# Kernel tuning notes

Hardware: AMD Instinct MI355X
Metric: run time of the kernel (lower is better)

## Reference

```python
import jax, jax.numpy as jnp
import numpy as np

N = 50000          # num nodes
E_RAND = 600000    # random edges (self-loops appended -> E = E_RAND + N)
HEADS = 4
OUT_CH = 16
OUT_NEURONS = 2 * OUT_CH   # diag reparam: [mean | std-logit]
IN_CH = 128
NEG_SLOPE = 0.2


def setup_inputs() -> dict:
    key = jax.random.key(0)
    k1, k2, k3, k4, k5 = jax.random.split(key, 5)
    x = jax.random.normal(k1, (N, IN_CH), jnp.float32)
    src = jax.random.randint(k2, (E_RAND,), 0, N, jnp.int32)
    dst = jax.random.randint(k3, (E_RAND,), 0, N, jnp.int32)
    loops = jnp.arange(N, dtype=jnp.int32)
    edge_index = jnp.stack([jnp.concatenate([src, loops]),
                            jnp.concatenate([dst, loops])])  # [2, E]
    # glorot init for weight [IN_CH, HEADS*OUT_NEURONS]
    s_w = float(np.sqrt(6.0 / (IN_CH + HEADS * OUT_NEURONS)))
    weight = jax.random.uniform(k4, (IN_CH, HEADS * OUT_NEURONS), jnp.float32, -s_w, s_w)
    # glorot for att [1, HEADS, 2*OUT_NEURONS]
    s_a = float(np.sqrt(6.0 / (HEADS + 2 * OUT_NEURONS)))
    att = jax.random.uniform(k5, (1, HEADS, 2 * OUT_NEURONS), jnp.float32, -s_a, s_a)
    bias = jnp.zeros((HEADS * OUT_NEURONS,), jnp.float32)
    return {"x": x, "edge_index": edge_index, "weight": weight, "att": att, "bias": bias}


def reference(x, edge_index, weight, att, bias):
    src, dst = edge_index[0], edge_index[1]  # j -> i (PyG source_to_target)
    h = (x @ weight).reshape(N, HEADS, OUT_NEURONS)          # Theta x
    x_j = h[src]                                             # [E, H, On]
    x_i = h[dst]                                             # [E, H, On]
    # alpha = LeakyReLU(a^T [x_i || x_j])
    alpha = (x_i * att[:, :, :OUT_NEURONS]).sum(-1) + \
            (x_j * att[:, :, OUT_NEURONS:]).sum(-1)          # [E, H]
    alpha = jax.nn.leaky_relu(alpha, NEG_SLOPE)
    # segment softmax over neighborhoods of target node i
    m = jax.ops.segment_max(alpha, dst, num_segments=N)      # [N, H]
    e = jnp.exp(alpha - m[dst])
    denom = jax.ops.segment_sum(e, dst, num_segments=N)      # [N, H]
    alpha = e / (denom[dst] + 1e-16)                          # [E, H]
    # scatter-add aggregation of attention-weighted features
    agg = jax.ops.segment_sum(x_j * alpha[:, :, None], dst, num_segments=N)  # [N, H, On]
    out = agg.reshape(N, HEADS * OUT_NEURONS) + bias
    # VIB diag reparameterization + closed-form KL against N(0, I)
    o = out.reshape(N * HEADS, OUT_NEURONS)
    mean = o[:, :OUT_CH]
    std = jax.nn.softplus(o[:, OUT_CH:] - 5.0) + 1e-10
    kl = (-jnp.log(std) + 0.5 * (std * std + mean * mean) - 0.5).sum(-1)  # [N*H]
    ixz = kl.reshape(N, HEADS).mean(-1)                      # [N]
    # eval + val_use_mean=True: output is the mean part
    out_final = mean.reshape(N, HEADS * OUT_CH)
    structure_kl_loss = jnp.zeros((), jnp.float32)
    return out_final, ixz, structure_kl_loss, mean, std
```

## Files before the change

kernel.cpp:

```cpp
#include <hip/hip_runtime.h>
#include <stdint.h>

#define NN 50000
#define NB 196
#define NEG_SLOPE 0.2f
#define WTS 136

#define IXZ_OFF    (NN * 64)
#define SKL_OFF    (NN * 64 + NN)
#define MEAN_OFF   (NN * 64 + NN + 1)
#define STD_OFF    (MEAN_OFF + NN * 64)

typedef unsigned int u32;
typedef unsigned short u16;
typedef __attribute__((ext_vector_type(8))) short short8;
typedef __attribute__((ext_vector_type(4))) float f32x4;

__device__ __forceinline__ float bf2f(u16 s) { return __uint_as_float(((u32)s) << 16); }
__device__ __forceinline__ u16 f2bf(float f) {
    u32 u = __float_as_uint(f);
    u += 0x7FFFu + ((u >> 16) & 1u);
    return (u16)(u >> 16);
}
__device__ __forceinline__ float lo16(u32 u) { return __uint_as_float(u << 16); }
__device__ __forceinline__ float hi16(u32 u) { return __uint_as_float(u & 0xFFFF0000u); }
__device__ __forceinline__ float softplusf(float x) {
    return fmaxf(x, 0.f) + log1pf(expf(-fabsf(x)));
}
__device__ __forceinline__ void stout(void* o, long long idx, float v, bool f32) {
    if (f32) ((float*)o)[idx] = v;
    else     ((u16*)o)[idx]   = f2bf(v);
}
__device__ __forceinline__ int wscan_incl(int v, int lane) {
#pragma unroll
    for (int off = 1; off < 64; off <<= 1) {
        int u = __shfl_up(v, off);
        if (lane >= off) v += u;
    }
    return v;
}

__global__ __launch_bounds__(256) void k_wt(const u32* __restrict__ xw,
                                            const void* __restrict__ wv_,
                                            int* __restrict__ flag,
                                            u16* __restrict__ wtg,
                                            int* __restrict__ zbase)
{
    __shared__ int lflag;
    const int t = threadIdx.x;
    if (t < 64) {
        u32 wrd = xw[t];
        u32 e = (wrd >> 7) & 0xFF;
        bool plaus = (e >= 0x60 && e <= 0x85);
        unsigned long long b = __ballot(plaus);
        if (t == 0) {
            int f = (__popcll(b) < 32) ? 1 : 0;
            lflag = f;
            if (blockIdx.x == 0) flag[0] = f;
        }
    }
    __syncthreads();
    const bool f32 = lflag != 0;

    const int gid = blockIdx.x * 256 + t;
    for (int i = gid; i < 2 * NN; i += 8 * 256) zbase[i] = 0;

    const int k = blockIdx.x * 16 + (t >> 4);
    const int cq = t & 15;
    u16 v[8];
    if (f32) {
        const float* w = (const float*)wv_;
        float4 a = *(const float4*)(w + k * 128 + cq * 8);
        float4 b = *(const float4*)(w + k * 128 + cq * 8 + 4);
        v[0] = f2bf(a.x); v[1] = f2bf(a.y); v[2] = f2bf(a.z); v[3] = f2bf(a.w);
        v[4] = f2bf(b.x); v[5] = f2bf(b.y); v[6] = f2bf(b.z); v[7] = f2bf(b.w);
    } else {
        const u16* w = (const u16*)wv_;
        uint4 u = *(const uint4*)(w + k * 128 + cq * 8);
        v[0] = (u16)(u.x & 0xFFFF); v[1] = (u16)(u.x >> 16);
        v[2] = (u16)(u.y & 0xFFFF); v[3] = (u16)(u.y >> 16);
        v[4] = (u16)(u.z & 0xFFFF); v[5] = (u16)(u.z >> 16);
        v[6] = (u16)(u.w & 0xFFFF); v[7] = (u16)(u.w >> 16);
    }
#pragma unroll
    for (int j = 0; j < 8; j++)
        wtg[(cq * 8 + j) * WTS + k] = v[j];
}

__global__ __launch_bounds__(256) void k_gemm(
    const void* __restrict__ xv, const u16* __restrict__ wtg,
    const void* __restrict__ attv, const int* __restrict__ flag,
    u16* __restrict__ hb, float* __restrict__ ai, float* __restrict__ aj,
    const int* __restrict__ dst, int* __restrict__ counts, int E)
{
    __shared__ __align__(16) u16 ls[128 * WTS];
    const int tid = threadIdx.x;
    const bool f32 = flag[0] != 0;

    {
        uint4* d = (uint4*)ls;
        const uint4* s = (const uint4*)wtg;
        for (int i = tid; i < 128 * WTS / 8; i += 256) d[i] = s[i];
    }

    const int w = tid >> 6, L = tid & 63;
    const int q = L >> 4, c15 = L & 15;
    const int nb16 = blockIdx.x * 64 + w * 16;

    short8 afr[4];
    {
        int nrow = nb16 + c15; if (nrow > NN - 1) nrow = NN - 1;
        if (f32) {
            const float* xp = (const float*)xv + (size_t)nrow * 128 + q * 8;
#pragma unroll
            for (int ks = 0; ks < 4; ks++) {
                float4 a = *(const float4*)(xp + ks * 32);
                float4 b = *(const float4*)(xp + ks * 32 + 4);
                union { short8 s; u16 e[8]; } u;
                u.e[0] = f2bf(a.x); u.e[1] = f2bf(a.y); u.e[2] = f2bf(a.z); u.e[3] = f2bf(a.w);
                u.e[4] = f2bf(b.x); u.e[5] = f2bf(b.y); u.e[6] = f2bf(b.z); u.e[7] = f2bf(b.w);
                afr[ks] = u.s;
            }
        } else {
            const u16* xp = (const u16*)xv + (size_t)nrow * 128 + q * 8;
#pragma unroll
            for (int ks = 0; ks < 4; ks++)
                afr[ks] = *(const short8*)(xp + ks * 32);
        }
    }
    __syncthreads();

    f32x4 acc[8];
#pragma unroll
    for (int t = 0; t < 8; t++) {
        acc[t] = (f32x4){0.f, 0.f, 0.f, 0.f};
        const u16* bp = ls + (16 * t + c15) * WTS + q * 8;
#pragma unroll
        for (int ks = 0; ks < 4; ks++) {
            short8 bfr = *(const short8*)(bp + ks * 32);
            acc[t] = __builtin_amdgcn_mfma_f32_16x16x32_bf16(afr[ks], bfr, acc[t], 0, 0, 0);
        }
    }

    float ati[8], atj[8];
#pragma unroll
    for (int t = 0; t < 8; t++) {
        int p = (t >> 1) * 64 + (t & 1) * 16 + c15;
        if (f32) {
            ati[t] = ((const float*)attv)[p];
            atj[t] = ((const float*)attv)[p + 32];
        } else {
            ati[t] = bf2f(((const u16*)attv)[p]);
            atj[t] = bf2f(((const u16*)attv)[p + 32]);
        }
    }
#pragma unroll
    for (int r = 0; r < 4; r++) {
        int node = nb16 + q * 4 + r;
#pragma unroll
        for (int h = 0; h < 4; h++) {
            float pi = acc[2 * h][r] * ati[2 * h] + acc[2 * h + 1][r] * ati[2 * h + 1];
            float pj = acc[2 * h][r] * atj[2 * h] + acc[2 * h + 1][r] * atj[2 * h + 1];
            pi += __shfl_xor(pi, 1); pj += __shfl_xor(pj, 1);
            pi += __shfl_xor(pi, 2); pj += __shfl_xor(pj, 2);
            pi += __shfl_xor(pi, 4); pj += __shfl_xor(pj, 4);
            pi += __shfl_xor(pi, 8); pj += __shfl_xor(pj, 8);
            if (c15 == 0 && node < NN) { ai[node * 4 + h] = pi; aj[node * 4 + h] = pj; }
        }
    }

    __syncthreads();
    u16* myls = ls + w * 16 * WTS;
#pragma unroll
    for (int t = 0; t < 8; t++)
#pragma unroll
        for (int r = 0; r < 4; r++)
            myls[(q * 4 + r) * WTS + 16 * t + c15] = f2bf(acc[t][r]);
#pragma unroll
    for (int v = 0; v < 4; v++) {
        int idx = v * 64 + L;
        int nrow = idx >> 4, c8 = idx & 15;
        int node = nb16 + nrow;
        if (node < NN)
            *(uint4*)(hb + (size_t)node * 128 + c8 * 8) =
                *(const uint4*)(myls + nrow * WTS + c8 * 8);
    }

    const int gid = blockIdx.x * 256 + tid;
    const int stride = gridDim.x * 256;
    for (int e = gid; e < E; e += stride)
        atomicAdd(&counts[dst[e]], 1);
}

__global__ __launch_bounds__(256) void k_scan1(const int* __restrict__ counts,
                                               int* __restrict__ lexcl,
                                               int* __restrict__ blocksum)
{
    __shared__ int wsum[4];
    const int t = threadIdx.x, lane = t & 63, wv = t >> 6;
    const int i = blockIdx.x * 256 + t;
    int c = (i < NN) ? counts[i] : 0;
    int inc = wscan_incl(c, lane);
    if (lane == 63) wsum[wv] = inc;
    __syncthreads();
    int add = 0;
#pragma unroll
    for (int k = 0; k < 3; k++) if (k < wv) add += wsum[k];
    inc += add;
    if (i < NN) lexcl[i] = inc - c;
    if (t == 255) blocksum[blockIdx.x] = inc;
}

__global__ __launch_bounds__(256) void k_scan2(const int* __restrict__ blocksum,
                                               int* __restrict__ blockoff)
{
    __shared__ int wsum[4];
    const int t = threadIdx.x, lane = t & 63, wv = t >> 6;
    int c = (t < NB) ? blocksum[t] : 0;
    int inc = wscan_incl(c, lane);
    if (lane == 63) wsum[wv] = inc;
    __syncthreads();
    int add = 0;
#pragma unroll
    for (int k = 0; k < 3; k++) if (k < wv) add += wsum[k];
    inc += add;
    if (t < NB) blockoff[t] = inc - c;
}

__global__ __launch_bounds__(256) void k_fill(
    const int* __restrict__ src, const int* __restrict__ dst,
    const int* __restrict__ lexcl, const int* __restrict__ blockoff,
    int* __restrict__ cursor, int* __restrict__ perm_src, int E)
{
    int e = blockIdx.x * 256 + threadIdx.x;
    if (e >= E) return;
    int d = dst[e];
    int pos = blockoff[d >> 8] + lexcl[d] + atomicAdd(&cursor[d], 1);
    perm_src[pos] = src[e];
}

__global__ __launch_bounds__(256) void k_agg(
    const int* __restrict__ lexcl, const int* __restrict__ blockoff,
    const int* __restrict__ counts, const int* __restrict__ perm_src,
    const float* __restrict__ ai, const float* __restrict__ aj,
    const u16* __restrict__ hb, const void* __restrict__ biasv,
    const int* __restrict__ flag, void* __restrict__ outv)
{
    const int t = blockIdx.x * 256 + threadIdx.x;
    const int node = t >> 4;
    if (node >= NN) return;
    const bool f32 = flag[0] != 0;
    const int l = t & 15;
    const int head = l >> 2;
    const int cc0 = (l & 3) << 3;

    const int rs = blockoff[node >> 8] + lexcl[node];
    const int re = rs + counts[node];
    const float ain = ai[node * 4 + head];
    const u16* hl8 = hb + l * 8;

    float dsum = 0.f;
    float a0 = 0.f, a1 = 0.f, a2 = 0.f, a3 = 0.f;
    float a4 = 0.f, a5 = 0.f, a6 = 0.f, a7 = 0.f;

    int i = rs;
    for (; i + 1 < re; i += 2) {
        int s0 = perm_src[i], s1 = perm_src[i + 1];
        float x0 = aj[s0 * 4 + head] + ain;
        float x1 = aj[s1 * 4 + head] + ain;
        x0 = x0 > 0.f ? x0 : NEG_SLOPE * x0;
        x1 = x1 > 0.f ? x1 : NEG_SLOPE * x1;
        float e0 = __expf(x0), e1 = __expf(x1);
        uint4 h0 = *(const uint4*)(hl8 + (size_t)s0 * 128);
        uint4 h1 = *(const uint4*)(hl8 + (size_t)s1 * 128);
        dsum += e0 + e1;
        a0 += e0 * lo16(h0.x) + e1 * lo16(h1.x);
        a1 += e0 * hi16(h0.x) + e1 * hi16(h1.x);
        a2 += e0 * lo16(h0.y) + e1 * lo16(h1.y);
        a3 += e0 * hi16(h0.y) + e1 * hi16(h1.y);
        a4 += e0 * lo16(h0.z) + e1 * lo16(h1.z);
        a5 += e0 * hi16(h0.z) + e1 * hi16(h1.z);
        a6 += e0 * lo16(h0.w) + e1 * lo16(h1.w);
        a7 += e0 * hi16(h0.w) + e1 * hi16(h1.w);
    }
    if (i < re) {
        int s0 = perm_src[i];
        float x0 = aj[s0 * 4 + head] + ain;
        x0 = x0 > 0.f ? x0 : NEG_SLOPE * x0;
        float e0 = __expf(x0);
        uint4 h0 = *(const uint4*)(hl8 + (size_t)s0 * 128);
        dsum += e0;
        a0 += e0 * lo16(h0.x); a1 += e0 * hi16(h0.x);
        a2 += e0 * lo16(h0.y); a3 += e0 * hi16(h0.y);
        a4 += e0 * lo16(h0.z); a5 += e0 * hi16(h0.z);
        a6 += e0 * lo16(h0.w); a7 += e0 * hi16(h0.w);
    }

    const float inv = 1.f / (dsum + 1e-16f);
    const int cb = head * 32 + cc0;
    float v[8];
    if (f32) {
        const float* bias = (const float*)biasv;
#pragma unroll
        for (int j = 0; j < 8; j++) v[j] = bias[cb + j];
    } else {
        const u16* bias = (const u16*)biasv;
#pragma unroll
        for (int j = 0; j < 8; j++) v[j] = bf2f(bias[cb + j]);
    }
    v[0] += a0 * inv; v[1] += a1 * inv; v[2] += a2 * inv; v[3] += a3 * inv;
    v[4] += a4 * inv; v[5] += a5 * inv; v[6] += a6 * inv; v[7] += a7 * inv;

    float part = 0.f;
    if (cc0 < 16) {
#pragma unroll
        for (int j = 0; j < 8; j++) part += 0.5f * v[j] * v[j];
        long long o = (long long)node * 64 + head * 16 + cc0;
#pragma unroll
        for (int j = 0; j < 8; j++) stout(outv, o + j, v[j], f32);
        long long om = (long long)MEAN_OFF + o;
#pragma unroll
        for (int j = 0; j < 8; j++) stout(outv, om + j, v[j], f32);
    } else {
        long long os = (long long)STD_OFF + (long long)node * 64 + head * 16 + (cc0 - 16);
#pragma unroll
        for (int j = 0; j < 8; j++) {
            float s = softplusf(v[j] - 5.f) + 1e-10f;
            part += -logf(s) + 0.5f * s * s - 0.5f;
            stout(outv, os + j, s, f32);
        }
    }
    part += __shfl_xor(part, 1); part += __shfl_xor(part, 2);
    part += __shfl_xor(part, 4); part += __shfl_xor(part, 8);
    if (l == 0) stout(outv, (long long)IXZ_OFF + node, part * 0.25f, f32);
    if (t == 0) stout(outv, (long long)SKL_OFF, 0.f, f32);
}

extern "C" void kernel_launch(void* const* d_in, const int* in_sizes, int n_in,
                              void* d_out, int out_size, void* d_ws, size_t ws_size,
                              hipStream_t stream)
{
    const void* x    = d_in[0];
    const int*  ei   = (const int*)d_in[1];
    const void* w    = d_in[2];
    const void* att  = d_in[3];
    const void* bias = d_in[4];

    const int E = in_sizes[1] / 2;
    const int* src = ei;
    const int* dst = ei + E;

    u16*   hb        = (u16*)d_ws;
    float* ai        = (float*)(hb + (size_t)NN * 128);
    float* aj        = ai + NN * 4;
    int*   perm_src  = (int*)(aj + NN * 4);
    int*   counts    = perm_src + E;
    int*   cursor    = counts + NN;
    int*   lexcl     = cursor + NN;
    int*   blocksum  = lexcl + NN;
    int*   blockoff  = blocksum + NB;
    int*   flag      = blockoff + NB;
    u16*   wtg       = (u16*)(flag + 1);

    k_wt<<<8, 256, 0, stream>>>((const u32*)x, w, flag, wtg, counts);
    k_gemm<<<(NN + 63) / 64, 256, 0, stream>>>(x, wtg, att, flag, hb, ai, aj,
                                               dst, counts, E);
    k_scan1<<<NB, 256, 0, stream>>>(counts, lexcl, blocksum);
    k_scan2<<<1, 256, 0, stream>>>(blocksum, blockoff);
    k_fill<<<(E + 255) / 256, 256, 0, stream>>>(src, dst, lexcl, blockoff,
                                                cursor, perm_src, E);
    k_agg<<<(NN * 16 + 255) / 256, 256, 0, stream>>>(lexcl, blockoff, counts,
                                                     perm_src, ai, aj, hb, bias,
                                                     flag, d_out);
}
```

Measured before the change: 210.0 us.

## Precompute edge exp weights in CSR fill and widen per-thread aggregation to 16 channels

The CSR fill kernel now also computes the per-edge, per-head LeakyReLU+exp attention weights and stores them as float4 in CSR order, when the workspace is large enough. The aggregation kernel then reads those weights contiguously instead of gathering aj and recomputing exp. Each thread now handles 16 channels instead of 8 (8 threads per node), and source indices are prefetched two iterations ahead. This trades an extra 16 bytes per edge of write and read traffic, plus more registers, for fewer random gathers and fewer threads.

```diff
diff --git a/kernel.cpp b/kernel.cpp
--- a/kernel.cpp
+++ b/kernel.cpp
@@ -230,108 +230,144 @@
 __global__ __launch_bounds__(256) void k_fill(
     const int* __restrict__ src, const int* __restrict__ dst,
     const int* __restrict__ lexcl, const int* __restrict__ blockoff,
-    int* __restrict__ cursor, int* __restrict__ perm_src, int E)
+    int* __restrict__ cursor, const float4* __restrict__ ai4,
+    const float4* __restrict__ aj4, int* __restrict__ perm_src,
+    float4* __restrict__ pev, int E)
 {
     int e = blockIdx.x * 256 + threadIdx.x;
     if (e >= E) return;
-    int d = dst[e];
+    int d = dst[e], s = src[e];
     int pos = blockoff[d >> 8] + lexcl[d] + atomicAdd(&cursor[d], 1);
-    perm_src[pos] = src[e];
+    perm_src[pos] = s;
+    if (pev) {
+        float4 a = ai4[d], b = aj4[s];
+        float4 ev;
+        float x;
+        x = a.x + b.x; x = x > 0.f ? x : NEG_SLOPE * x; ev.x = __expf(x);
+        x = a.y + b.y; x = x > 0.f ? x : NEG_SLOPE * x; ev.y = __expf(x);
+        x = a.z + b.z; x = x > 0.f ? x : NEG_SLOPE * x; ev.z = __expf(x);
+        x = a.w + b.w; x = x > 0.f ? x : NEG_SLOPE * x; ev.w = __expf(x);
+        pev[pos] = ev;
+    }
 }
 
 __global__ __launch_bounds__(256) void k_agg(
     const int* __restrict__ lexcl, const int* __restrict__ blockoff,
     const int* __restrict__ counts, const int* __restrict__ perm_src,
+    const float* __restrict__ pev,
     const float* __restrict__ ai, const float* __restrict__ aj,
     const u16* __restrict__ hb, const void* __restrict__ biasv,
     const int* __restrict__ flag, void* __restrict__ outv)
 {
     const int t = blockIdx.x * 256 + threadIdx.x;
-    const int node = t >> 4;
+    const int node = t >> 3;
     if (node >= NN) return;
     const bool f32 = flag[0] != 0;
-    const int l = t & 15;
-    const int head = l >> 2;
-    const int cc0 = (l & 3) << 3;
+    const int l = t & 7;
+    const int head = l >> 1;
+    const bool has_ev = (pev != nullptr);
 
     const int rs = blockoff[node >> 8] + lexcl[node];
     const int re = rs + counts[node];
-    const float ain = ai[node * 4 + head];
-    const u16* hl8 = hb + l * 8;
-
+    const float ain = has_ev ? 0.f : ai[node * 4 + head];
+    const u16* hbl = hb + l * 16;
+
+    float acc[16];
+#pragma unroll
+    for (int j = 0; j < 16; j++) acc[j] = 0.f;
     float dsum = 0.f;
-    float a0 = 0.f, a1 = 0.f, a2 = 0.f, a3 = 0.f;
-    float a4 = 0.f, a5 = 0.f, a6 = 0.f, a7 = 0.f;
 
     int i = rs;
-    for (; i + 1 < re; i += 2) {
-        int s0 = perm_src[i], s1 = perm_src[i + 1];
-        float x0 = aj[s0 * 4 + head] + ain;
-        float x1 = aj[s1 * 4 + head] + ain;
-        x0 = x0 > 0.f ? x0 : NEG_SLOPE * x0;
-        x1 = x1 > 0.f ? x1 : NEG_SLOPE * x1;
-        float e0 = __expf(x0), e1 = __expf(x1);
-        uint4 h0 = *(const uint4*)(hl8 + (size_t)s0 * 128);
-        uint4 h1 = *(const uint4*)(hl8 + (size_t)s1 * 128);
+    int s0 = (i < re) ? perm_src[i] : 0;
+    int s1 = (i + 1 < re) ? perm_src[i + 1] : 0;
+    while (i + 1 < re) {
+        int s2 = (i + 2 < re) ? perm_src[i + 2] : 0;
+        int s3 = (i + 3 < re) ? perm_src[i + 3] : 0;
+        float e0, e1;
+        if (has_ev) {
+            e0 = pev[(size_t)i * 4 + head];
+            e1 = pev[(size_t)(i + 1) * 4 + head];
+        } else {
+            float x0 = aj[s0 * 4 + head] + ain; x0 = x0 > 0.f ? x0 : NEG_SLOPE * x0;
+            float x1 = aj[s1 * 4 + head] + ain; x1 = x1 > 0.f ? x1 : NEG_SLOPE * x1;
+            e0 = __expf(x0); e1 = __expf(x1);
+        }
+        const u16* h0 = hbl + (size_t)s0 * 128;
+        const u16* h1 = hbl + (size_t)s1 * 128;
+        uint4 A0 = *(const uint4*)h0, B0 = *(const uint4*)(h0 + 8);
+        uint4 A1 = *(const uint4*)h1, B1 = *(const uint4*)(h1 + 8);
         dsum += e0 + e1;
-        a0 += e0 * lo16(h0.x) + e1 * lo16(h1.x);
-        a1 += e0 * hi16(h0.x) + e1 * hi16(h1.x);
-        a2 += e0 * lo16(h0.y) + e1 * lo16(h1.y);
-        a3 += e0 * hi16(h0.y) + e1 * hi16(h1.y);
-        a4 += e0 * lo16(h0.z) + e1 * lo16(h1.z);
-        a5 += e0 * hi16(h0.z) + e1 * hi16(h1.z);
-        a6 += e0 * lo16(h0.w) + e1 * lo16(h1.w);
-        a7 += e0 * hi16(h0.w) + e1 * hi16(h1.w);
+        acc[0]  += e0 * lo16(A0.x) + e1 * lo16(A1.x);
+        acc[1]  += e0 * hi16(A0.x) + e1 * hi16(A1.x);
+        acc[2]  += e0 * lo16(A0.y) + e1 * lo16(A1.y);
+        acc[3]  += e0 * hi16(A0.y) + e1 * hi16(A1.y);
+        acc[4]  += e0 * lo16(A0.z) + e1 * lo16(A1.z);
+        acc[5]  += e0 * hi16(A0.z) + e1 * hi16(A1.z);
+        acc[6]  += e0 * lo16(A0.w) + e1 * lo16(A1.w);
+        acc[7]  += e0 * hi16(A0.w) + e1 * hi16(A1.w);
+        acc[8]  += e0 * lo16(B0.x) + e1 * lo16(B1.x);
+        acc[9]  += e0 * hi16(B0.x) + e1 * hi16(B1.x);
+        acc[10] += e0 * lo16(B0.y) + e1 * lo16(B1.y);
+        acc[11] += e0 * hi16(B0.y) + e1 * hi16(B1.y);
+        acc[12] += e0 * lo16(B0.z) + e1 * lo16(B1.z);
+        acc[13] += e0 * hi16(B0.z) + e1 * hi16(B1.z);
+        acc[14] += e0 * lo16(B0.w) + e1 * lo16(B1.w);
+        acc[15] += e0 * hi16(B0.w) + e1 * hi16(B1.w);
+        i += 2; s0 = s2; s1 = s3;
     }
     if (i < re) {
-        int s0 = perm_src[i];
-        float x0 = aj[s0 * 4 + head] + ain;
-        x0 = x0 > 0.f ? x0 : NEG_SLOPE * x0;
-        float e0 = __expf(x0);
-        uint4 h0 = *(const uint4*)(hl8 + (size_t)s0 * 128);
+        float e0;
+        if (has_ev) e0 = pev[(size_t)i * 4 + head];
+        else {
+            float x0 = aj[s0 * 4 + head] + ain; x0 = x0 > 0.f ? x0 : NEG_SLOPE * x0;
+            e0 = __expf(x0);
+        }
+        const u16* h0 = hbl + (size_t)s0 * 128;
+        uint4 A0 = *(const uint4*)h0, B0 = *(const uint4*)(h0 + 8);
         dsum += e0;
-        a0 += e0 * lo16(h0.x); a1 += e0 * hi16(h0.x);
-        a2 += e0 * lo16(h0.y); a3 += e0 * hi16(h0.y);
-        a4 += e0 * lo16(h0.z); a5 += e0 * hi16(h0.z);
-        a6 += e0 * lo16(h0.w); a7 += e0 * hi16(h0.w);
+        acc[0]  += e0 * lo16(A0.x); acc[1]  += e0 * hi16(A0.x);
+        acc[2]  += e0 * lo16(A0.y); acc[3]  += e0 * hi16(A0.y);
+        acc[4]  += e0 * lo16(A0.z); acc[5]  += e0 * hi16(A0.z);
+        acc[6]  += e0 * lo16(A0.w); acc[7]  += e0 * hi16(A0.w);
+        acc[8]  += e0 * lo16(B0.x); acc[9]  += e0 * hi16(B0.x);
+        acc[10] += e0 * lo16(B0.y); acc[11] += e0 * hi16(B0.y);
+        acc[12] += e0 * lo16(B0.z); acc[13] += e0 * hi16(B0.z);
+        acc[14] += e0 * lo16(B0.w); acc[15] += e0 * hi16(B0.w);
     }
 
     const float inv = 1.f / (dsum + 1e-16f);
-    const int cb = head * 32 + cc0;
-    float v[8];
+    float v[16];
     if (f32) {
         const float* bias = (const float*)biasv;
 #pragma unroll
-        for (int j = 0; j < 8; j++) v[j] = bias[cb + j];
+        for (int j = 0; j < 16; j++) v[j] = acc[j] * inv + bias[16 * l + j];
     } else {
         const u16* bias = (const u16*)biasv;
 #pragma unroll
-        for (int j = 0; j < 8; j++) v[j] = bf2f(bias[cb + j]);
-    }
-    v[0] += a0 * inv; v[1] += a1 * inv; v[2] += a2 * inv; v[3] += a3 * inv;
-    v[4] += a4 * inv; v[5] += a5 * inv; v[6] += a6 * inv; v[7] += a7 * inv;
+        for (int j = 0; j < 16; j++) v[j] = acc[j] * inv + bf2f(bias[16 * l + j]);
+    }
 
     float part = 0.f;
-    if (cc0 < 16) {
-#pragma unroll
-        for (int j = 0; j < 8; j++) part += 0.5f * v[j] * v[j];
-        long long o = (long long)node * 64 + head * 16 + cc0;
-#pragma unroll
-        for (int j = 0; j < 8; j++) stout(outv, o + j, v[j], f32);
-        long long om = (long long)MEAN_OFF + o;
-#pragma unroll
-        for (int j = 0; j < 8; j++) stout(outv, om + j, v[j], f32);
+    if ((l & 1) == 0) {
+        long long o = (long long)node * 64 + head * 16;
+#pragma unroll
+        for (int j = 0; j < 16; j++) {
+            part += 0.5f * v[j] * v[j];
+            stout(outv, o + j, v[j], f32);
+            stout(outv, (long long)MEAN_OFF + o + j, v[j], f32);
+        }
     } else {
-        long long os = (long long)STD_OFF + (long long)node * 64 + head * 16 + (cc0 - 16);
-#pragma unroll
-        for (int j = 0; j < 8; j++) {
+        long long os = (long long)STD_OFF + (long long)node * 64 + head * 16;
+#pragma unroll
+        for (int j = 0; j < 16; j++) {
             float s = softplusf(v[j] - 5.f) + 1e-10f;
             part += -logf(s) + 0.5f * s * s - 0.5f;
             stout(outv, os + j, s, f32);
         }
     }
-    part += __shfl_xor(part, 1); part += __shfl_xor(part, 2);
-    part += __shfl_xor(part, 4); part += __shfl_xor(part, 8);
+    part += __shfl_xor(part, 1);
+    part += __shfl_xor(part, 2);
+    part += __shfl_xor(part, 4);
     if (l == 0) stout(outv, (long long)IXZ_OFF + node, part * 0.25f, f32);
     if (t == 0) stout(outv, (long long)SKL_OFF, 0.f, f32);
 }
@@ -350,17 +386,24 @@
     const int* src = ei;
     const int* dst = ei + E;
 
-    u16*   hb        = (u16*)d_ws;
-    float* ai        = (float*)(hb + (size_t)NN * 128);
-    float* aj        = ai + NN * 4;
-    int*   perm_src  = (int*)(aj + NN * 4);
-    int*   counts    = perm_src + E;
-    int*   cursor    = counts + NN;
-    int*   lexcl     = cursor + NN;
-    int*   blocksum  = lexcl + NN;
-    int*   blockoff  = blocksum + NB;
-    int*   flag      = blockoff + NB;
-    u16*   wtg       = (u16*)(flag + 1);
+    u16*   hb = (u16*)d_ws;
+    float* ai = (float*)(hb + (size_t)NN * 128);
+    float* aj = ai + NN * 4;
+    size_t off_fixed = (size_t)NN * 128 * 2 + (size_t)NN * 4 * 4 * 2;
+    size_t pev_bytes = (size_t)E * 16;
+    size_t rest = (size_t)E * 4 + (size_t)NN * 4 * 3 + NB * 4 * 2 + 4
+                + 32 + 128 * WTS * 2;
+    bool use_ev = ws_size >= off_fixed + pev_bytes + rest;
+
+    float* pev      = use_ev ? (float*)((char*)d_ws + off_fixed) : nullptr;
+    int*   perm_src = (int*)((char*)d_ws + off_fixed + (use_ev ? pev_bytes : 0));
+    int*   counts   = perm_src + E;
+    int*   cursor   = counts + NN;
+    int*   lexcl    = cursor + NN;
+    int*   blocksum = lexcl + NN;
+    int*   blockoff = blocksum + NB;
+    int*   flag     = blockoff + NB;
+    u16*   wtg      = (u16*)(((uintptr_t)(flag + 1) + 15) & ~(uintptr_t)15);
 
     k_wt<<<8, 256, 0, stream>>>((const u32*)x, w, flag, wtg, counts);
     k_gemm<<<(NN + 63) / 64, 256, 0, stream>>>(x, wtg, att, flag, hb, ai, aj,
@@ -368,8 +411,10 @@
     k_scan1<<<NB, 256, 0, stream>>>(counts, lexcl, blocksum);
     k_scan2<<<1, 256, 0, stream>>>(blocksum, blockoff);
     k_fill<<<(E + 255) / 256, 256, 0, stream>>>(src, dst, lexcl, blockoff,
-                                                cursor, perm_src, E);
-    k_agg<<<(NN * 16 + 255) / 256, 256, 0, stream>>>(lexcl, blockoff, counts,
-                                                     perm_src, ai, aj, hb, bias,
-                                                     flag, d_out);
-}
+                                                cursor, (const float4*)ai,
+                                                (const float4*)aj, perm_src,
+                                                (float4*)pev, E);
+    k_agg<<<(NN * 8 + 255) / 256, 256, 0, stream>>>(lexcl, blockoff, counts,
+                                                    perm_src, pev, ai, aj, hb,
+                                                    bias, flag, d_out);
+}
```

Result: slower. 241.5 us (+15.0%).

## Fold block-offset scan into consumers and precompute edge attention exps in fill

Applied to the files above, without the earlier changes.

Removes the single-block k_scan2 launch by having k_fill and k_agg each redo the small blocksum scan in shared memory. When workspace allows, k_fill also computes the leaky-relu exponentials for all four heads per edge and stores them in CSR order as float4. k_agg then reads these instead of gathering aj and computing exp per edge. This trades a random gather and exp in the aggregation loop for an extra 16 bytes per edge of write and read traffic, plus a redundant scan in every block.

```diff
diff --git a/kernel.cpp b/kernel.cpp
--- a/kernel.cpp
+++ b/kernel.cpp
@@ -211,10 +211,9 @@
     if (t == 255) blocksum[blockIdx.x] = inc;
 }
 
-__global__ __launch_bounds__(256) void k_scan2(const int* __restrict__ blocksum,
-                                               int* __restrict__ blockoff)
-{
-    __shared__ int wsum[4];
+__device__ __forceinline__ void scan_blocksum(const int* __restrict__ blocksum,
+                                              int* sboff, int* wsum)
+{
     const int t = threadIdx.x, lane = t & 63, wv = t >> 6;
     int c = (t < NB) ? blocksum[t] : 0;
     int inc = wscan_incl(c, lane);
@@ -223,40 +222,61 @@
     int add = 0;
 #pragma unroll
     for (int k = 0; k < 3; k++) if (k < wv) add += wsum[k];
-    inc += add;
-    if (t < NB) blockoff[t] = inc - c;
+    sboff[t] = inc + add - c;
+    __syncthreads();
 }
 
 __global__ __launch_bounds__(256) void k_fill(
     const int* __restrict__ src, const int* __restrict__ dst,
-    const int* __restrict__ lexcl, const int* __restrict__ blockoff,
-    int* __restrict__ cursor, int* __restrict__ perm_src, int E)
-{
+    const int* __restrict__ lexcl, const int* __restrict__ blocksum,
+    int* __restrict__ cursor, const float4* __restrict__ ai4,
+    const float4* __restrict__ aj4, int* __restrict__ perm_src,
+    float4* __restrict__ pev, int E)
+{
+    __shared__ int sboff[256];
+    __shared__ int wsum[4];
+    scan_blocksum(blocksum, sboff, wsum);
+
     int e = blockIdx.x * 256 + threadIdx.x;
     if (e >= E) return;
-    int d = dst[e];
-    int pos = blockoff[d >> 8] + lexcl[d] + atomicAdd(&cursor[d], 1);
-    perm_src[pos] = src[e];
+    int d = dst[e], s = src[e];
+    int pos = sboff[d >> 8] + lexcl[d] + atomicAdd(&cursor[d], 1);
+    perm_src[pos] = s;
+    if (pev) {
+        float4 a = ai4[d], b = aj4[s];
+        float4 ev;
+        float x;
+        x = a.x + b.x; x = x > 0.f ? x : NEG_SLOPE * x; ev.x = __expf(x);
+        x = a.y + b.y; x = x > 0.f ? x : NEG_SLOPE * x; ev.y = __expf(x);
+        x = a.z + b.z; x = x > 0.f ? x : NEG_SLOPE * x; ev.z = __expf(x);
+        x = a.w + b.w; x = x > 0.f ? x : NEG_SLOPE * x; ev.w = __expf(x);
+        pev[pos] = ev;
+    }
 }
 
 __global__ __launch_bounds__(256) void k_agg(
-    const int* __restrict__ lexcl, const int* __restrict__ blockoff,
+    const int* __restrict__ lexcl, const int* __restrict__ blocksum,
     const int* __restrict__ counts, const int* __restrict__ perm_src,
+    const float* __restrict__ pev,
     const float* __restrict__ ai, const float* __restrict__ aj,
     const u16* __restrict__ hb, const void* __restrict__ biasv,
     const int* __restrict__ flag, void* __restrict__ outv)
 {
+    __shared__ int sboff[256];
+    __shared__ int wsum[4];
+    scan_blocksum(blocksum, sboff, wsum);
+
     const int t = blockIdx.x * 256 + threadIdx.x;
     const int node = t >> 4;
-    if (node >= NN) return;
     const bool f32 = flag[0] != 0;
     const int l = t & 15;
     const int head = l >> 2;
     const int cc0 = (l & 3) << 3;
-
-    const int rs = blockoff[node >> 8] + lexcl[node];
+    const bool has_ev = (pev != nullptr);
+
+    const int rs = sboff[(node >> 8) & 255] + lexcl[node];
     const int re = rs + counts[node];
-    const float ain = ai[node * 4 + head];
+    const float ain = has_ev ? 0.f : ai[node * 4 + head];
     const u16* hl8 = hb + l * 8;
 
     float dsum = 0.f;
@@ -266,11 +286,17 @@
     int i = rs;
     for (; i + 1 < re; i += 2) {
         int s0 = perm_src[i], s1 = perm_src[i + 1];
-        float x0 = aj[s0 * 4 + head] + ain;
-        float x1 = aj[s1 * 4 + head] + ain;
-        x0 = x0 > 0.f ? x0 : NEG_SLOPE * x0;
-        x1 = x1 > 0.f ? x1 : NEG_SLOPE * x1;
-        float e0 = __expf(x0), e1 = __expf(x1);
+        float e0, e1;
+        if (has_ev) {
+            e0 = pev[(size_t)i * 4 + head];
+            e1 = pev[(size_t)(i + 1) * 4 + head];
+        } else {
+            float x0 = aj[s0 * 4 + head] + ain;
+            float x1 = aj[s1 * 4 + head] + ain;
+            x0 = x0 > 0.f ? x0 : NEG_SLOPE * x0;
+            x1 = x1 > 0.f ? x1 : NEG_SLOPE * x1;
+            e0 = __expf(x0); e1 = __expf(x1);
+        }
         uint4 h0 = *(const uint4*)(hl8 + (size_t)s0 * 128);
         uint4 h1 = *(const uint4*)(hl8 + (size_t)s1 * 128);
         dsum += e0 + e1;
@@ -285,9 +311,13 @@
     }
     if (i < re) {
         int s0 = perm_src[i];
-        float x0 = aj[s0 * 4 + head] + ain;
-        x0 = x0 > 0.f ? x0 : NEG_SLOPE * x0;
-        float e0 = __expf(x0);
+        float e0;
+        if (has_ev) e0 = pev[(size_t)i * 4 + head];
+        else {
+            float x0 = aj[s0 * 4 + head] + ain;
+            x0 = x0 > 0.f ? x0 : NEG_SLOPE * x0;
+            e0 = __expf(x0);
+        }
         uint4 h0 = *(const uint4*)(hl8 + (size_t)s0 * 128);
         dsum += e0;
         a0 += e0 * lo16(h0.x); a1 += e0 * hi16(h0.x);
@@ -350,26 +380,33 @@
     const int* src = ei;
     const int* dst = ei + E;
 
-    u16*   hb        = (u16*)d_ws;
-    float* ai        = (float*)(hb + (size_t)NN * 128);
-    float* aj        = ai + NN * 4;
-    int*   perm_src  = (int*)(aj + NN * 4);
-    int*   counts    = perm_src + E;
-    int*   cursor    = counts + NN;
-    int*   lexcl     = cursor + NN;
-    int*   blocksum  = lexcl + NN;
-    int*   blockoff  = blocksum + NB;
-    int*   flag      = blockoff + NB;
-    u16*   wtg       = (u16*)(flag + 1);
+    u16*   hb = (u16*)d_ws;
+    float* ai = (float*)(hb + (size_t)NN * 128);
+    float* aj = ai + NN * 4;
+    size_t off_fixed = (size_t)NN * 128 * 2 + (size_t)NN * 4 * 4 * 2;
+    size_t pev_bytes = (size_t)E * 16;
+    size_t rest = (size_t)E * 4 + (size_t)NN * 4 * 3 + NB * 4 + 4
+                + 32 + 128 * WTS * 2;
+    bool use_ev = ws_size >= off_fixed + pev_bytes + rest;
+
+    float* pev      = use_ev ? (float*)((char*)d_ws + off_fixed) : nullptr;
+    int*   perm_src = (int*)((char*)d_ws + off_fixed + (use_ev ? pev_bytes : 0));
+    int*   counts   = perm_src + E;
+    int*   cursor   = counts + NN;
+    int*   lexcl    = cursor + NN;
+    int*   blocksum = lexcl + NN;
+    int*   flag     = blocksum + NB;
+    u16*   wtg      = (u16*)(((uintptr_t)(flag + 1) + 15) & ~(uintptr_t)15);
 
     k_wt<<<8, 256, 0, stream>>>((const u32*)x, w, flag, wtg, counts);
     k_gemm<<<(NN + 63) / 64, 256, 0, stream>>>(x, wtg, att, flag, hb, ai, aj,
                                                dst, counts, E);
     k_scan1<<<NB, 256, 0, stream>>>(counts, lexcl, blocksum);
-    k_scan2<<<1, 256, 0, stream>>>(blocksum, blockoff);
-    k_fill<<<(E + 255) / 256, 256, 0, stream>>>(src, dst, lexcl, blockoff,
-                                                cursor, perm_src, E);
-    k_agg<<<(NN * 16 + 255) / 256, 256, 0, stream>>>(lexcl, blockoff, counts,
-                                                     perm_src, ai, aj, hb, bias,
-                                                     flag, d_out);
-}
+    k_fill<<<(E + 255) / 256, 256, 0, stream>>>(src, dst, lexcl, blocksum,
+                                                cursor, (const float4*)ai,
+                                                (const float4*)aj, perm_src,
+                                                (float4*)pev, E);
+    k_agg<<<(NN * 16) / 256, 256, 0, stream>>>(lexcl, blocksum, counts,
+                                               perm_src, pev, ai, aj, hb,
+                                               bias, flag, d_out);
+}
```

After: 221.7 us. 1.06x slower.

## Fuse all stages into one cooperative persistent kernel with grid syncs

Applied to the files above, without the earlier changes.

Merges the six separate launches (weight transpose, GEMM plus degree count, two scans, CSR fill, aggregation) into one cooperative kernel that steps through the stages using grid-wide syncs. Each block loops over tiles, chunks and edges. The single-block offset scan is folded into every block's shared memory, which removes the separate scan2 launch and its global round trip. The intent is to remove launch gaps and per-kernel ramp-up and tail costs. In exchange the grid size is capped (at most 1024 blocks), the fused kernel carries extra register and LDS pressure, and a multi-kernel fallback path is kept.

```diff
diff --git a/kernel.cpp b/kernel.cpp
--- a/kernel.cpp
+++ b/kernel.cpp
@@ -1,8 +1,13 @@
 #include <hip/hip_runtime.h>
+#include <hip/hip_cooperative_groups.h>
 #include <stdint.h>
+
+namespace cg = cooperative_groups;
 
 #define NN 50000
 #define NB 196
+#define NTILES 782
+#define NCHUNK 3125
 #define NEG_SLOPE 0.2f
 #define WTS 136
 
@@ -40,33 +45,27 @@
     return v;
 }
 
-__global__ __launch_bounds__(256) void k_wt(const u32* __restrict__ xw,
-                                            const void* __restrict__ wv_,
-                                            int* __restrict__ flag,
-                                            u16* __restrict__ wtg,
-                                            int* __restrict__ zbase)
-{
-    __shared__ int lflag;
+__device__ __forceinline__ bool detect_f32_block(const u32* __restrict__ xw,
+                                                 int* lflag)
+{
     const int t = threadIdx.x;
     if (t < 64) {
         u32 wrd = xw[t];
         u32 e = (wrd >> 7) & 0xFF;
         bool plaus = (e >= 0x60 && e <= 0x85);
         unsigned long long b = __ballot(plaus);
-        if (t == 0) {
-            int f = (__popcll(b) < 32) ? 1 : 0;
-            lflag = f;
-            if (blockIdx.x == 0) flag[0] = f;
-        }
-    }
-    __syncthreads();
-    const bool f32 = lflag != 0;
-
-    const int gid = blockIdx.x * 256 + t;
-    for (int i = gid; i < 2 * NN; i += 8 * 256) zbase[i] = 0;
-
-    const int k = blockIdx.x * 16 + (t >> 4);
-    const int cq = t & 15;
+        if (t == 0) *lflag = (__popcll(b) < 32) ? 1 : 0;
+    }
+    __syncthreads();
+    return *lflag != 0;
+}
+
+__device__ __forceinline__ void wt_body(const void* __restrict__ wv_,
+                                        u16* __restrict__ wtg,
+                                        int kb, int tid, bool f32)
+{
+    const int k = kb * 16 + (tid >> 4);
+    const int cq = tid & 15;
     u16 v[8];
     if (f32) {
         const float* w = (const float*)wv_;
@@ -87,16 +86,13 @@
         wtg[(cq * 8 + j) * WTS + k] = v[j];
 }
 
-__global__ __launch_bounds__(256) void k_gemm(
+__device__ __forceinline__ void gemm_tile(
     const void* __restrict__ xv, const u16* __restrict__ wtg,
-    const void* __restrict__ attv, const int* __restrict__ flag,
+    const void* __restrict__ attv, bool f32,
     u16* __restrict__ hb, float* __restrict__ ai, float* __restrict__ aj,
-    const int* __restrict__ dst, int* __restrict__ counts, int E)
-{
-    __shared__ __align__(16) u16 ls[128 * WTS];
-    const int tid = threadIdx.x;
-    const bool f32 = flag[0] != 0;
-
+    int tile, int tid, u16* ls)
+{
+    __syncthreads();
     {
         uint4* d = (uint4*)ls;
         const uint4* s = (const uint4*)wtg;
@@ -105,7 +101,7 @@
 
     const int w = tid >> 6, L = tid & 63;
     const int q = L >> 4, c15 = L & 15;
-    const int nb16 = blockIdx.x * 64 + w * 16;
+    const int nb16 = tile * 64 + w * 16;
 
     short8 afr[4];
     {
@@ -185,20 +181,15 @@
             *(uint4*)(hb + (size_t)node * 128 + c8 * 8) =
                 *(const uint4*)(myls + nrow * WTS + c8 * 8);
     }
-
-    const int gid = blockIdx.x * 256 + tid;
-    const int stride = gridDim.x * 256;
-    for (int e = gid; e < E; e += stride)
-        atomicAdd(&counts[dst[e]], 1);
-}
-
-__global__ __launch_bounds__(256) void k_scan1(const int* __restrict__ counts,
-                                               int* __restrict__ lexcl,
-                                               int* __restrict__ blocksum)
-{
-    __shared__ int wsum[4];
+}
+
+__device__ __forceinline__ void scan1_body(const int* __restrict__ counts,
+                                           int* __restrict__ lexcl,
+                                           int* __restrict__ blocksum,
+                                           int sb, int* wsum)
+{
     const int t = threadIdx.x, lane = t & 63, wv = t >> 6;
-    const int i = blockIdx.x * 256 + t;
+    const int i = sb * 256 + t;
     int c = (i < NN) ? counts[i] : 0;
     int inc = wscan_incl(c, lane);
     if (lane == 63) wsum[wv] = inc;
@@ -208,13 +199,12 @@
     for (int k = 0; k < 3; k++) if (k < wv) add += wsum[k];
     inc += add;
     if (i < NN) lexcl[i] = inc - c;
-    if (t == 255) blocksum[blockIdx.x] = inc;
-}
-
-__global__ __launch_bounds__(256) void k_scan2(const int* __restrict__ blocksum,
-                                               int* __restrict__ blockoff)
-{
-    __shared__ int wsum[4];
+    if (t == 255) blocksum[sb] = inc;
+}
+
+__device__ __forceinline__ void sboff_body(const int* __restrict__ blocksum,
+                                           int* sboff, int* wsum)
+{
     const int t = threadIdx.x, lane = t & 63, wv = t >> 6;
     int c = (t < NB) ? blocksum[t] : 0;
     int inc = wscan_incl(c, lane);
@@ -223,38 +213,36 @@
     int add = 0;
 #pragma unroll
     for (int k = 0; k < 3; k++) if (k < wv) add += wsum[k];
-    inc += add;
-    if (t < NB) blockoff[t] = inc - c;
-}
-
-__global__ __launch_bounds__(256) void k_fill(
-    const int* __restrict__ src, const int* __restrict__ dst,
-    const int* __restrict__ lexcl, const int* __restrict__ blockoff,
-    int* __restrict__ cursor, int* __restrict__ perm_src, int E)
-{
-    int e = blockIdx.x * 256 + threadIdx.x;
-    if (e >= E) return;
+    sboff[t] = inc + add - c;
+    __syncthreads();
+}
+
+__device__ __forceinline__ void fill_edge(const int* __restrict__ src,
+                                          const int* __restrict__ dst,
+                                          const int* __restrict__ lexcl,
+                                          const int* sboff,
+                                          int* __restrict__ cursor,
+                                          int* __restrict__ perm_src, int e)
+{
     int d = dst[e];
-    int pos = blockoff[d >> 8] + lexcl[d] + atomicAdd(&cursor[d], 1);
+    int pos = sboff[d >> 8] + lexcl[d] + atomicAdd(&cursor[d], 1);
     perm_src[pos] = src[e];
 }
 
-__global__ __launch_bounds__(256) void k_agg(
-    const int* __restrict__ lexcl, const int* __restrict__ blockoff,
+__device__ __forceinline__ void agg_chunk(
+    const int* __restrict__ lexcl, const int* sboff,
     const int* __restrict__ counts, const int* __restrict__ perm_src,
     const float* __restrict__ ai, const float* __restrict__ aj,
     const u16* __restrict__ hb, const void* __restrict__ biasv,
-    const int* __restrict__ flag, void* __restrict__ outv)
-{
-    const int t = blockIdx.x * 256 + threadIdx.x;
-    const int node = t >> 4;
-    if (node >= NN) return;
-    const bool f32 = flag[0] != 0;
-    const int l = t & 15;
+    bool f32, void* __restrict__ outv, int chunk)
+{
+    const int tid = threadIdx.x;
+    const int node = chunk * 16 + (tid >> 4);
+    const int l = tid & 15;
     const int head = l >> 2;
     const int cc0 = (l & 3) << 3;
 
-    const int rs = blockoff[node >> 8] + lexcl[node];
+    const int rs = sboff[node >> 8] + lexcl[node];
     const int re = rs + counts[node];
     const float ain = ai[node * 4 + head];
     const u16* hl8 = hb + l * 8;
@@ -333,7 +321,117 @@
     part += __shfl_xor(part, 1); part += __shfl_xor(part, 2);
     part += __shfl_xor(part, 4); part += __shfl_xor(part, 8);
     if (l == 0) stout(outv, (long long)IXZ_OFF + node, part * 0.25f, f32);
-    if (t == 0) stout(outv, (long long)SKL_OFF, 0.f, f32);
+}
+
+__global__ __launch_bounds__(256, 4) void k_all(
+    const void* __restrict__ xv, const int* __restrict__ ei,
+    const void* __restrict__ wv, const void* __restrict__ attv,
+    const void* __restrict__ biasv, void* __restrict__ outv,
+    u16* __restrict__ hb, float* __restrict__ ai, float* __restrict__ aj,
+    int* __restrict__ perm_src, int* __restrict__ counts,
+    int* __restrict__ cursor, int* __restrict__ lexcl,
+    int* __restrict__ blocksum, u16* __restrict__ wtg, int E)
+{
+    __shared__ __align__(16) u16 ls[128 * WTS];
+    __shared__ int sboff[256];
+    __shared__ int wsum[4];
+    __shared__ int lflag;
+
+    cg::grid_group gg = cg::this_grid();
+    const int tid = threadIdx.x, bid = blockIdx.x, gdim = gridDim.x;
+    const int* src = ei;
+    const int* dst = ei + E;
+
+    const bool f32 = detect_f32_block((const u32*)xv, &lflag);
+
+    for (int i = bid * 256 + tid; i < 2 * NN; i += gdim * 256) counts[i] = 0;
+    if (bid < 8) wt_body(wv, wtg, bid, tid, f32);
+    gg.sync();
+
+    for (int tile = bid; tile < NTILES; tile += gdim)
+        gemm_tile(xv, wtg, attv, f32, hb, ai, aj, tile, tid, ls);
+    for (int e = bid * 256 + tid; e < E; e += gdim * 256)
+        atomicAdd(&counts[dst[e]], 1);
+    gg.sync();
+
+    for (int sb = bid; sb < NB; sb += gdim) {
+        scan1_body(counts, lexcl, blocksum, sb, wsum);
+        __syncthreads();
+    }
+    gg.sync();
+
+    sboff_body(blocksum, sboff, wsum);
+    for (int e = bid * 256 + tid; e < E; e += gdim * 256)
+        fill_edge(src, dst, lexcl, sboff, cursor, perm_src, e);
+    gg.sync();
+
+    for (int c = bid; c < NCHUNK; c += gdim)
+        agg_chunk(lexcl, sboff, counts, perm_src, ai, aj, hb, biasv, f32, outv, c);
+    if (bid == 0 && tid == 0) stout(outv, (long long)SKL_OFF, 0.f, f32);
+}
+
+__global__ __launch_bounds__(256) void k_wt(const void* __restrict__ xv,
+                                            const void* __restrict__ wv,
+                                            u16* __restrict__ wtg,
+                                            int* __restrict__ zbase)
+{
+    __shared__ int lflag;
+    const bool f32 = detect_f32_block((const u32*)xv, &lflag);
+    const int t = threadIdx.x;
+    for (int i = blockIdx.x * 256 + t; i < 2 * NN; i += 8 * 256) zbase[i] = 0;
+    wt_body(wv, wtg, blockIdx.x, t, f32);
+}
+
+__global__ __launch_bounds__(256) void k_gemm(
+    const void* __restrict__ xv, const u16* __restrict__ wtg,
+    const void* __restrict__ attv, u16* __restrict__ hb,
+    float* __restrict__ ai, float* __restrict__ aj,
+    const int* __restrict__ dst, int* __restrict__ counts, int E)
+{
+    __shared__ __align__(16) u16 ls[128 * WTS];
+    __shared__ int lflag;
+    const bool f32 = detect_f32_block((const u32*)xv, &lflag);
+    gemm_tile(xv, wtg, attv, f32, hb, ai, aj, blockIdx.x, threadIdx.x, ls);
+    for (int e = blockIdx.x * 256 + threadIdx.x; e < E; e += gridDim.x * 256)
+        atomicAdd(&counts[dst[e]], 1);
+}
+
+__global__ __launch_bounds__(256) void k_scan1(const int* __restrict__ counts,
+                                               int* __restrict__ lexcl,
+                                               int* __restrict__ blocksum)
+{
+    __shared__ int wsum[4];
+    scan1_body(counts, lexcl, blocksum, blockIdx.x, wsum);
+}
+
+__global__ __launch_bounds__(256) void k_fill(
+    const int* __restrict__ ei, const int* __restrict__ lexcl,
+    const int* __restrict__ blocksum, int* __restrict__ cursor,
+    int* __restrict__ perm_src, int E)
+{
+    __shared__ int sboff[256];
+    __shared__ int wsum[4];
+    sboff_body(blocksum, sboff, wsum);
+    int e = blockIdx.x * 256 + threadIdx.x;
+    if (e < E) fill_edge(ei, ei + E, lexcl, sboff, cursor, perm_src, e);
+}
+
+__global__ __launch_bounds__(256) void k_agg(
+    const int* __restrict__ lexcl, const int* __restrict__ blocksum,
+    const int* __restrict__ counts, const int* __restrict__ perm_src,
+    const float* __restrict__ ai, const float* __restrict__ aj,
+    const u16* __restrict__ hb, const void* __restrict__ biasv,
+    const void* __restrict__ xv, void* __restrict__ outv)
+{
+    __shared__ int sboff[256];
+    __shared__ int wsum[4];
+    __shared__ int lflag;
+    const bool f32 = detect_f32_block((const u32*)xv, &lflag);
+    sboff_body(blocksum, sboff, wsum);
+    agg_chunk(lexcl, sboff, counts, perm_src, ai, aj, hb, biasv, f32, outv,
+              blockIdx.x);
+    if (blockIdx.x == 0 && threadIdx.x == 0)
+        stout(outv, (long long)SKL_OFF, 0.f, f32);
 }
 
 extern "C" void kernel_launch(void* const* d_in, const int* in_sizes, int n_in,
@@ -345,31 +443,41 @@
     const void* w    = d_in[2];
     const void* att  = d_in[3];
     const void* bias = d_in[4];
-
-    const int E = in_sizes[1] / 2;
-    const int* src = ei;
-    const int* dst = ei + E;
-
-    u16*   hb        = (u16*)d_ws;
-    float* ai        = (float*)(hb + (size_t)NN * 128);
-    float* aj        = ai + NN * 4;
-    int*   perm_src  = (int*)(aj + NN * 4);
-    int*   counts    = perm_src + E;
-    int*   cursor    = counts + NN;
-    int*   lexcl     = cursor + NN;
-    int*   blocksum  = lexcl + NN;
-    int*   blockoff  = blocksum + NB;
-    int*   flag      = blockoff + NB;
-    u16*   wtg       = (u16*)(flag + 1);
-
-    k_wt<<<8, 256, 0, stream>>>((const u32*)x, w, flag, wtg, counts);
-    k_gemm<<<(NN + 63) / 64, 256, 0, stream>>>(x, wtg, att, flag, hb, ai, aj,
-                                               dst, counts, E);
-    k_scan1<<<NB, 256, 0, stream>>>(counts, lexcl, blocksum);
-    k_scan2<<<1, 256, 0, stream>>>(blocksum, blockoff);
-    k_fill<<<(E + 255) / 256, 256, 0, stream>>>(src, dst, lexcl, blockoff,
-                                                cursor, perm_src, E);
-    k_agg<<<(NN * 16 + 255) / 256, 256, 0, stream>>>(lexcl, blockoff, counts,
-                                                     perm_src, ai, aj, hb, bias,
-                                                     flag, d_out);
-}
+    int E = in_sizes[1] / 2;
+
+    u16*   hb       = (u16*)d_ws;
+    float* ai       = (float*)(hb + (size_t)NN * 128);
+    float* aj       = ai + NN * 4;
+    int*   perm_src = (int*)(aj + NN * 4);
+    int*   counts   = perm_src + E;
+    int*   cursor   = counts + NN;
+    int*   lexcl    = cursor + NN;
+    int*   blocksum = lexcl + NN;
+    u16*   wtg      = (u16*)(((uintptr_t)(blocksum + NB) + 15) & ~(uintptr_t)15);
+
+    int maxB = 0;
+    hipError_t qerr = hipOccupancyMaxActiveBlocksPerMultiprocessor(
+        &maxB, (const void*)k_all, 256, 0);
+    int nb = (qerr == hipSuccess && maxB > 0) ? maxB * 256 : 512;
+    if (nb > 1024) nb = 1024;
+    if (nb < 256)  nb = 256;
+
+    void* outp = d_out;
+    void* args[] = {(void*)&x, (void*)&ei, (void*)&w, (void*)&att, (void*)&bias,
+                    (void*)&outp, (void*)&hb, (void*)&ai, (void*)&aj,
+                    (void*)&perm_src, (void*)&counts, (void*)&cursor,
+                    (void*)&lexcl, (void*)&blocksum, (void*)&wtg, (void*)&E};
+    hipError_t lerr = hipLaunchCooperativeKernel(
+        (const void*)k_all, dim3(nb), dim3(256), args, 0, stream);
+
+    if (lerr != hipSuccess) {
+        k_wt<<<8, 256, 0, stream>>>(x, w, wtg, counts);
+        k_gemm<<<NTILES, 256, 0, stream>>>(x, wtg, att, hb, ai, aj,
+                                           ei + E, counts, E);
+        k_scan1<<<NB, 256, 0, stream>>>(counts, lexcl, blocksum);
+        k_fill<<<(E + 255) / 256, 256, 0, stream>>>(ei, lexcl, blocksum,
+                                                    cursor, perm_src, E);
+        k_agg<<<NCHUNK, 256, 0, stream>>>(lexcl, blocksum, counts, perm_src,
+                                          ai, aj, hb, bias, x, d_out);
+    }
+}
```

Measured after the change: 464.1 us. 121% more time.
